# Kernel tuning notes

Measured on AMD Instinct MI355X. Metric: run time of the kernel, lower is better.

The kernel has to match this reference:

```python
import jax, jax.numpy as jnp
import numpy as np

N_NODES = 100000
N_EDGES = 1600000
DIMS = [64, 64, 64, 32]  # in -> hid -> hid -> out


def setup_inputs() -> dict:
    key = jax.random.key(0)
    ks = jax.random.split(key, 12)
    features = jax.random.normal(ks[0], (N_NODES, DIMS[0]), dtype=jnp.float32)
    edge_weights = jax.random.uniform(ks[1], (N_EDGES,), dtype=jnp.float32)
    src = jax.random.randint(ks[2], (N_EDGES,), 0, N_NODES, dtype=jnp.int32)
    dst = jax.random.randint(ks[3], (N_EDGES,), 0, N_NODES, dtype=jnp.int32)
    def lin(kw, kb, i, o):
        s = 1.0 / np.sqrt(i)
        W = jax.random.uniform(kw, (i, o), minval=-s, maxval=s, dtype=jnp.float32)
        b = jax.random.uniform(kb, (o,), minval=-s, maxval=s, dtype=jnp.float32)
        return W, b
    W1, b1 = lin(ks[4], ks[5], DIMS[0], DIMS[1])
    W2, b2 = lin(ks[6], ks[7], DIMS[1], DIMS[2])
    Wp, bp = lin(ks[8], ks[9], DIMS[2], DIMS[3])
    return {"features": features, "edge_weights": edge_weights, "src": src,
            "dst": dst, "W1": W1, "b1": b1, "W2": W2, "b2": b2,
            "Wp": Wp, "bp": bp}


def _graph_conv(x, src, dst, ew, W, b, norm_src, norm_dst):
    # DGL GraphConv, norm='both', with edge weights:
    # h = D_in^{-1/2} * A_w * (D_out^{-1/2} * x) @ W + b
    h = x * norm_src[:, None]
    msg = h[src] * ew[:, None]                      # [E, d] gather + edge-weight
    agg = jax.ops.segment_sum(msg, dst, num_segments=N_NODES)  # scatter-sum
    agg = agg * norm_dst[:, None]
    return agg @ W + b


def reference(features, edge_weights, src, dst, W1, b1, W2, b2, Wp, bp):
    ones = jnp.ones((N_EDGES,), dtype=features.dtype)
    out_deg = jax.ops.segment_sum(ones, src, num_segments=N_NODES)
    in_deg = jax.ops.segment_sum(ones, dst, num_segments=N_NODES)
    norm_src = jnp.power(jnp.clip(out_deg, 1.0, None), -0.5)
    norm_dst = jnp.power(jnp.clip(in_deg, 1.0, None), -0.5)

    x = jax.nn.relu(_graph_conv(features, src, dst, edge_weights, W1, b1, norm_src, norm_dst))
    x = jax.nn.relu(_graph_conv(x, src, dst, edge_weights, W2, b2, norm_src, norm_dst))
    x = _graph_conv(x, src, dst, edge_weights, Wp, bp, norm_src, norm_dst)
    return x
```

## Files before the change

kernel.cpp:

```cpp
#include <hip/hip_runtime.h>

#define N_NODES 100000
#define N_EDGES 1600000
#define NB_SCAN 391
#define NSLICE 64
#define SLICE_E 25000
#define NBUCK 4
#define BUCK_N 25000
#define BUCK_W 12500

__device__ __forceinline__ unsigned short f2bf(float f) {
    unsigned int u = __float_as_uint(f);
    return (unsigned short)((u + 0x7FFFu + ((u >> 16) & 1u)) >> 16);
}
__device__ __forceinline__ float bf2f(unsigned short b) {
    return __uint_as_float(((unsigned int)b) << 16);
}


template <bool RANK>
__global__ void __launch_bounds__(512) count_kernel(
        const int* __restrict__ ids,
        unsigned short* __restrict__ slicecnt,
        unsigned short* __restrict__ rank16) {
    __shared__ unsigned int cnt[BUCK_W];
    int s = blockIdx.x >> 2;
    int b = blockIdx.x & 3;
    int b0 = b * BUCK_N;
    for (int w = threadIdx.x; w < BUCK_W; w += 512) cnt[w] = 0;
    __syncthreads();
    int base = s * SLICE_E;
    for (int i = threadIdx.x; i < SLICE_E; i += 512) {
        int e = base + i;
        int id = ids[e] - b0;
        if ((unsigned)id < (unsigned)BUCK_N) {
            unsigned int shift = (id & 1) * 16;
            unsigned int old = atomicAdd(&cnt[id >> 1], 1u << shift);
            if (RANK) rank16[e] = (unsigned short)((old >> shift) & 0xFFFFu);
        }
    }
    __syncthreads();
    unsigned int* row = (unsigned int*)(slicecnt + (size_t)s * N_NODES) + b * BUCK_W;
    for (int w = threadIdx.x; w < BUCK_W; w += 512) row[w] = cnt[w];
}

__global__ void scan_slices_kernel(unsigned short* __restrict__ scd,
                                   const unsigned short* __restrict__ scs,
                                   int* __restrict__ deg_int,
                                   float* __restrict__ norm_dst,
                                   float* __restrict__ norm_src) {
    int n = blockIdx.x * blockDim.x + threadIdx.x;
    if (n >= N_NODES) return;
    unsigned int tot = 0;
    for (int s = 0; s < NSLICE; ++s) {
        size_t idx = (size_t)s * N_NODES + n;
        unsigned int c = scd[idx];
        scd[idx] = (unsigned short)tot;
        tot += c;
    }
    deg_int[n] = (int)tot;
    norm_dst[n] = rsqrtf(fmaxf((float)tot, 1.0f));
    unsigned int so = 0;
    for (int s = 0; s < NSLICE; ++s) so += scs[(size_t)s * N_NODES + n];
    norm_src[n] = rsqrtf(fmaxf((float)so, 1.0f));
}


__global__ void block_sum_kernel(const int* __restrict__ deg_in, int* __restrict__ block_sums) {
    __shared__ int sdata[256];
    int t = threadIdx.x;
    int n = blockIdx.x * 256 + t;
    int v = (n < N_NODES) ? deg_in[n] : 0;
    sdata[t] = v;
    __syncthreads();
    for (int off = 128; off > 0; off >>= 1) {
        if (t < off) sdata[t] += sdata[t + off];
        __syncthreads();
    }
    if (t == 0) block_sums[blockIdx.x] = sdata[0];
}

__global__ void scan_blocks_kernel(const int* __restrict__ block_sums, int* __restrict__ block_off) {
    __shared__ int part[512];
    int t = threadIdx.x;
    int v = (t < NB_SCAN) ? block_sums[t] : 0;
    part[t] = v;
    __syncthreads();
    for (int off = 1; off < 512; off <<= 1) {
        int u = (t >= off) ? part[t - off] : 0;
        __syncthreads();
        part[t] += u;
        __syncthreads();
    }
    if (t < NB_SCAN) block_off[t] = part[t] - v;
}

__global__ void scatter_rowptr_kernel(const int* __restrict__ deg_in,
                                      const int* __restrict__ block_off,
                                      int* __restrict__ row_ptr) {
    __shared__ int part[256];
    int t = threadIdx.x;
    int n = blockIdx.x * 256 + t;
    int v = (n < N_NODES) ? deg_in[n] : 0;
    part[t] = v;
    __syncthreads();
    for (int off = 1; off < 256; off <<= 1) {
        int u = (t >= off) ? part[t - off] : 0;
        __syncthreads();
        part[t] += u;
        __syncthreads();
    }
    int excl = part[t] - v + block_off[blockIdx.x];
    if (n < N_NODES) row_ptr[n] = excl;
    if (n == N_NODES - 1) row_ptr[N_NODES] = excl + v;
}


__global__ void fill_kernel(const int* __restrict__ src, const int* __restrict__ dst,
                            const float* __restrict__ ew,
                            const float* __restrict__ ns, const float* __restrict__ nd,
                            const int* __restrict__ row_ptr,
                            const unsigned short* __restrict__ sliceoff,
                            const unsigned short* __restrict__ rank16,
                            int2* __restrict__ epack) {
    int i = blockIdx.x * blockDim.x + threadIdx.x;
    int stride = gridDim.x * blockDim.x;
    for (int e = i; e < N_EDGES; e += stride) {
        int s = src[e], d = dst[e];
        int sl = e / SLICE_E;
        int slot = row_ptr[d] + (int)sliceoff[(size_t)sl * N_NODES + d] + (int)rank16[e];
        float c = ns[s] * ew[e] * nd[d];
        epack[slot] = make_int2(s, __float_as_int(c));
    }
}


template <int BM, int DOUT, bool BIAS_RELU>
__global__ void __launch_bounds__(256) matmul_kernel(
        const float* __restrict__ x, const float* __restrict__ W,
        const float* __restrict__ bin, unsigned short* __restrict__ h) {
    constexpr int S = 65;
    constexpr int CG = DOUT / 4;
    __shared__ float Xs[BM * S];
    __shared__ float Ws[64 * DOUT];
    int tid = threadIdx.x;
    int n0 = blockIdx.x * BM;

    for (int i = tid; i < 16 * DOUT; i += 256)
        ((float4*)Ws)[i] = ((const float4*)W)[i];

    float4 bv4;
    if (BIAS_RELU) bv4 = ((const float4*)bin)[tid & 15];
    int c0 = (tid & 15) * 4;
    for (int r = tid >> 4; r < BM; r += 16) {
        int n = n0 + r;
        int nc = n < N_NODES ? n : N_NODES - 1;
        float4 v = ((const float4*)(x + (size_t)nc * 64))[tid & 15];
        if (BIAS_RELU) {
            v.x = fmaxf(v.x + bv4.x, 0.0f);
            v.y = fmaxf(v.y + bv4.y, 0.0f);
            v.z = fmaxf(v.z + bv4.z, 0.0f);
            v.w = fmaxf(v.w + bv4.w, 0.0f);
        }
        Xs[r * S + c0]     = v.x;
        Xs[r * S + c0 + 1] = v.y;
        Xs[r * S + c0 + 2] = v.z;
        Xs[r * S + c0 + 3] = v.w;
    }
    __syncthreads();

    int cg = tid % CG;
    int ng = tid / CG;

    float acc[4][4];
#pragma unroll
    for (int i = 0; i < 4; ++i)
#pragma unroll
        for (int j = 0; j < 4; ++j) acc[i][j] = 0.0f;

#pragma unroll 16
    for (int k = 0; k < 64; ++k) {
        float4 wk = *(const float4*)(&Ws[k * DOUT + cg * 4]);
        float xk[4];
#pragma unroll
        for (int i = 0; i < 4; ++i) xk[i] = Xs[(ng * 4 + i) * S + k];
#pragma unroll
        for (int i = 0; i < 4; ++i) {
            acc[i][0] = fmaf(xk[i], wk.x, acc[i][0]);
            acc[i][1] = fmaf(xk[i], wk.y, acc[i][1]);
            acc[i][2] = fmaf(xk[i], wk.z, acc[i][2]);
            acc[i][3] = fmaf(xk[i], wk.w, acc[i][3]);
        }
    }

#pragma unroll
    for (int i = 0; i < 4; ++i) {
        int n = n0 + ng * 4 + i;
        if (n < N_NODES) {
            ushort4 o;
            o.x = f2bf(acc[i][0]); o.y = f2bf(acc[i][1]);
            o.z = f2bf(acc[i][2]); o.w = f2bf(acc[i][3]);
            *(ushort4*)(&h[(size_t)n * DOUT + cg * 4]) = o;
        }
    }
}


template <int D, bool FINAL>
__global__ void __launch_bounds__(256) csr_agg_kernel(
        const int* __restrict__ row_ptr,
        const int2* __restrict__ epack,
        const unsigned short* __restrict__ h,
        const float* __restrict__ bias, float* __restrict__ out) {
    int tid = blockIdx.x * blockDim.x + threadIdx.x;
    int stride = gridDim.x * blockDim.x;
    int lane = threadIdx.x & (D - 1);
    int node0 = tid / D;
    int nstride = stride / D;
    const unsigned short* hl = h + lane;
    for (int n = node0; n < N_NODES; n += nstride) {
        int s = row_ptr[n];
        int e = row_ptr[n + 1];
        float a0 = 0.f, a1 = 0.f, a2 = 0.f, a3 = 0.f;
        float a4 = 0.f, a5 = 0.f, a6 = 0.f, a7 = 0.f;
        int i = s;
        for (; i + 7 < e; i += 8) {
            int2 p0 = epack[i],     p1 = epack[i + 1], p2 = epack[i + 2], p3 = epack[i + 3];
            int2 p4 = epack[i + 4], p5 = epack[i + 5], p6 = epack[i + 6], p7 = epack[i + 7];
            float h0 = bf2f(hl[(size_t)p0.x * D]);
            float h1 = bf2f(hl[(size_t)p1.x * D]);
            float h2 = bf2f(hl[(size_t)p2.x * D]);
            float h3 = bf2f(hl[(size_t)p3.x * D]);
            float h4 = bf2f(hl[(size_t)p4.x * D]);
            float h5 = bf2f(hl[(size_t)p5.x * D]);
            float h6 = bf2f(hl[(size_t)p6.x * D]);
            float h7 = bf2f(hl[(size_t)p7.x * D]);
            a0 = fmaf(h0, __int_as_float(p0.y), a0);
            a1 = fmaf(h1, __int_as_float(p1.y), a1);
            a2 = fmaf(h2, __int_as_float(p2.y), a2);
            a3 = fmaf(h3, __int_as_float(p3.y), a3);
            a4 = fmaf(h4, __int_as_float(p4.y), a4);
            a5 = fmaf(h5, __int_as_float(p5.y), a5);
            a6 = fmaf(h6, __int_as_float(p6.y), a6);
            a7 = fmaf(h7, __int_as_float(p7.y), a7);
        }
        for (; i + 3 < e; i += 4) {
            int2 p0 = epack[i], p1 = epack[i + 1], p2 = epack[i + 2], p3 = epack[i + 3];
            a0 = fmaf(bf2f(hl[(size_t)p0.x * D]), __int_as_float(p0.y), a0);
            a1 = fmaf(bf2f(hl[(size_t)p1.x * D]), __int_as_float(p1.y), a1);
            a2 = fmaf(bf2f(hl[(size_t)p2.x * D]), __int_as_float(p2.y), a2);
            a3 = fmaf(bf2f(hl[(size_t)p3.x * D]), __int_as_float(p3.y), a3);
        }
        for (; i < e; ++i) {
            int2 p = epack[i];
            a0 = fmaf(bf2f(hl[(size_t)p.x * D]), __int_as_float(p.y), a0);
        }
        float acc = ((a0 + a1) + (a2 + a3)) + ((a4 + a5) + (a6 + a7));
        if (FINAL) out[(size_t)n * D + lane] = acc + bias[lane];
        else       out[(size_t)n * D + lane] = acc;
    }
}

extern "C" void kernel_launch(void* const* d_in, const int* in_sizes, int n_in,
                              void* d_out, int out_size, void* d_ws, size_t ws_size,
                              hipStream_t stream) {
    const float* features = (const float*)d_in[0];
    const float* ew       = (const float*)d_in[1];
    const int*   src      = (const int*)d_in[2];
    const int*   dst      = (const int*)d_in[3];
    const float* W1       = (const float*)d_in[4];
    const float* b1       = (const float*)d_in[5];
    const float* W2       = (const float*)d_in[6];
    const float* b2       = (const float*)d_in[7];
    const float* Wp       = (const float*)d_in[8];
    const float* bp       = (const float*)d_in[9];
    float* out = (float*)d_out;

    float* ws = (float*)d_ws;
    float* norm_src = ws;
    float* norm_dst = ws + 100000;
    int*   deg_int  = (int*)(ws + 200000);
    int*   row_ptr  = (int*)(ws + 300000);
    int*   block_sums = (int*)(ws + 400002);
    int*   block_off  = (int*)(ws + 400394);
    unsigned short* rank16 = (unsigned short*)(ws + 400800);
    int2*  epack = (int2*)(ws + 1200800);
    float* bufA  = ws + 4400800;
    unsigned short* hbuf = (unsigned short*)(ws + 10800800);

    unsigned short* slicecnt_dst = (unsigned short*)bufA;
    unsigned short* slicecnt_src = hbuf;

    count_kernel<true><<<NSLICE * NBUCK, 512, 0, stream>>>(dst, slicecnt_dst, rank16);
    count_kernel<false><<<NSLICE * NBUCK, 512, 0, stream>>>(src, slicecnt_src, nullptr);
    scan_slices_kernel<<<NB_SCAN, 256, 0, stream>>>(slicecnt_dst, slicecnt_src,
                                                    deg_int, norm_dst, norm_src);
    block_sum_kernel<<<NB_SCAN, 256, 0, stream>>>(deg_int, block_sums);
    scan_blocks_kernel<<<1, 512, 0, stream>>>(block_sums, block_off);
    scatter_rowptr_kernel<<<NB_SCAN, 256, 0, stream>>>(deg_int, block_off, row_ptr);
    fill_kernel<<<2048, 256, 0, stream>>>(src, dst, ew, norm_src, norm_dst,
                                          row_ptr, slicecnt_dst, rank16, epack);

    matmul_kernel<64, 64, false><<<1563, 256, 0, stream>>>(features, W1, nullptr, hbuf);
    csr_agg_kernel<64, false><<<4096, 256, 0, stream>>>(row_ptr, epack, hbuf, nullptr, bufA);

    matmul_kernel<64, 64, true><<<1563, 256, 0, stream>>>(bufA, W2, b1, hbuf);
    csr_agg_kernel<64, false><<<4096, 256, 0, stream>>>(row_ptr, epack, hbuf, nullptr, bufA);

    matmul_kernel<128, 32, true><<<782, 256, 0, stream>>>(bufA, Wp, b2, hbuf);
    csr_agg_kernel<32, true><<<4096, 256, 0, stream>>>(row_ptr, epack, hbuf, bp, out);
}
```

Baseline: 307.5 us.

## Fuse CSR aggregation with the following layer's bias, ReLU and matmul

```diff
diff --git a/kernel.cpp b/kernel.cpp
--- a/kernel.cpp
+++ b/kernel.cpp
@@ -135,10 +135,10 @@
 }
 
 
-template <int BM, int DOUT, bool BIAS_RELU>
+template <int BM, int DOUT>
 __global__ void __launch_bounds__(256) matmul_kernel(
         const float* __restrict__ x, const float* __restrict__ W,
-        const float* __restrict__ bin, unsigned short* __restrict__ h) {
+        unsigned short* __restrict__ h) {
     constexpr int S = 65;
     constexpr int CG = DOUT / 4;
     __shared__ float Xs[BM * S];
@@ -149,19 +149,11 @@
     for (int i = tid; i < 16 * DOUT; i += 256)
         ((float4*)Ws)[i] = ((const float4*)W)[i];
 
-    float4 bv4;
-    if (BIAS_RELU) bv4 = ((const float4*)bin)[tid & 15];
     int c0 = (tid & 15) * 4;
     for (int r = tid >> 4; r < BM; r += 16) {
         int n = n0 + r;
         int nc = n < N_NODES ? n : N_NODES - 1;
         float4 v = ((const float4*)(x + (size_t)nc * 64))[tid & 15];
-        if (BIAS_RELU) {
-            v.x = fmaxf(v.x + bv4.x, 0.0f);
-            v.y = fmaxf(v.y + bv4.y, 0.0f);
-            v.z = fmaxf(v.z + bv4.z, 0.0f);
-            v.w = fmaxf(v.w + bv4.w, 0.0f);
-        }
         Xs[r * S + c0]     = v.x;
         Xs[r * S + c0 + 1] = v.y;
         Xs[r * S + c0 + 2] = v.z;
@@ -171,7 +163,6 @@
 
     int cg = tid % CG;
     int ng = tid / CG;
-
     float acc[4][4];
 #pragma unroll
     for (int i = 0; i < 4; ++i)
@@ -206,7 +197,113 @@
 }
 
 
-template <int D, bool FINAL>
+template <int DOUT>
+__global__ void __launch_bounds__(512) agg_mm_kernel(
+        const int* __restrict__ row_ptr,
+        const int2* __restrict__ epack,
+        const unsigned short* __restrict__ hin,
+        const float* __restrict__ bias_in,
+        const float* __restrict__ W,
+        unsigned short* __restrict__ hout) {
+    constexpr int BM = 128;
+    constexpr int S = 65;
+    constexpr int CG = DOUT / 4;
+    constexpr int RI = BM * CG / 512;
+    __shared__ float Xs[BM * S];
+    __shared__ float Ws[64 * DOUT];
+    int tid = threadIdx.x;
+    int n0 = blockIdx.x * BM;
+
+    for (int i = tid; i < 16 * DOUT; i += 512)
+        ((float4*)Ws)[i] = ((const float4*)W)[i];
+
+    int lane = tid & 63;
+    int wid = tid >> 6;
+    float bv = bias_in[lane];
+    const unsigned short* hl = hin + lane;
+
+    for (int j = 0; j < 16; ++j) {
+        int n = n0 + wid * 16 + j;
+        float a0 = 0.f, a1 = 0.f, a2 = 0.f, a3 = 0.f;
+        float a4 = 0.f, a5 = 0.f, a6 = 0.f, a7 = 0.f;
+        if (n < N_NODES) {
+            int s = row_ptr[n];
+            int e = row_ptr[n + 1];
+            int i = s;
+            for (; i + 7 < e; i += 8) {
+                int2 p0 = epack[i],     p1 = epack[i + 1], p2 = epack[i + 2], p3 = epack[i + 3];
+                int2 p4 = epack[i + 4], p5 = epack[i + 5], p6 = epack[i + 6], p7 = epack[i + 7];
+                float h0 = bf2f(hl[(size_t)p0.x * 64]);
+                float h1 = bf2f(hl[(size_t)p1.x * 64]);
+                float h2 = bf2f(hl[(size_t)p2.x * 64]);
+                float h3 = bf2f(hl[(size_t)p3.x * 64]);
+                float h4 = bf2f(hl[(size_t)p4.x * 64]);
+                float h5 = bf2f(hl[(size_t)p5.x * 64]);
+                float h6 = bf2f(hl[(size_t)p6.x * 64]);
+                float h7 = bf2f(hl[(size_t)p7.x * 64]);
+                a0 = fmaf(h0, __int_as_float(p0.y), a0);
+                a1 = fmaf(h1, __int_as_float(p1.y), a1);
+                a2 = fmaf(h2, __int_as_float(p2.y), a2);
+                a3 = fmaf(h3, __int_as_float(p3.y), a3);
+                a4 = fmaf(h4, __int_as_float(p4.y), a4);
+                a5 = fmaf(h5, __int_as_float(p5.y), a5);
+                a6 = fmaf(h6, __int_as_float(p6.y), a6);
+                a7 = fmaf(h7, __int_as_float(p7.y), a7);
+            }
+            for (; i + 3 < e; i += 4) {
+                int2 p0 = epack[i], p1 = epack[i + 1], p2 = epack[i + 2], p3 = epack[i + 3];
+                a0 = fmaf(bf2f(hl[(size_t)p0.x * 64]), __int_as_float(p0.y), a0);
+                a1 = fmaf(bf2f(hl[(size_t)p1.x * 64]), __int_as_float(p1.y), a1);
+                a2 = fmaf(bf2f(hl[(size_t)p2.x * 64]), __int_as_float(p2.y), a2);
+                a3 = fmaf(bf2f(hl[(size_t)p3.x * 64]), __int_as_float(p3.y), a3);
+            }
+            for (; i < e; ++i) {
+                int2 p = epack[i];
+                a0 = fmaf(bf2f(hl[(size_t)p.x * 64]), __int_as_float(p.y), a0);
+            }
+        }
+        float acc = ((a0 + a1) + (a2 + a3)) + ((a4 + a5) + (a6 + a7));
+        Xs[(wid * 16 + j) * S + lane] = fmaxf(acc + bv, 0.0f);
+    }
+    __syncthreads();
+
+    int cg = tid % CG;
+    int ng = tid / CG;
+    float acc[RI][4];
+#pragma unroll
+    for (int i = 0; i < RI; ++i)
+#pragma unroll
+        for (int j = 0; j < 4; ++j) acc[i][j] = 0.0f;
+
+#pragma unroll 16
+    for (int k = 0; k < 64; ++k) {
+        float4 wk = *(const float4*)(&Ws[k * DOUT + cg * 4]);
+        float xk[RI];
+#pragma unroll
+        for (int i = 0; i < RI; ++i) xk[i] = Xs[(ng * RI + i) * S + k];
+#pragma unroll
+        for (int i = 0; i < RI; ++i) {
+            acc[i][0] = fmaf(xk[i], wk.x, acc[i][0]);
+            acc[i][1] = fmaf(xk[i], wk.y, acc[i][1]);
+            acc[i][2] = fmaf(xk[i], wk.z, acc[i][2]);
+            acc[i][3] = fmaf(xk[i], wk.w, acc[i][3]);
+        }
+    }
+
+#pragma unroll
+    for (int i = 0; i < RI; ++i) {
+        int n = n0 + ng * RI + i;
+        if (n < N_NODES) {
+            ushort4 o;
+            o.x = f2bf(acc[i][0]); o.y = f2bf(acc[i][1]);
+            o.z = f2bf(acc[i][2]); o.w = f2bf(acc[i][3]);
+            *(ushort4*)(&hout[(size_t)n * DOUT + cg * 4]) = o;
+        }
+    }
+}
+
+
+template <int D>
 __global__ void __launch_bounds__(256) csr_agg_kernel(
         const int* __restrict__ row_ptr,
         const int2* __restrict__ epack,
@@ -227,22 +324,14 @@
         for (; i + 7 < e; i += 8) {
             int2 p0 = epack[i],     p1 = epack[i + 1], p2 = epack[i + 2], p3 = epack[i + 3];
             int2 p4 = epack[i + 4], p5 = epack[i + 5], p6 = epack[i + 6], p7 = epack[i + 7];
-            float h0 = bf2f(hl[(size_t)p0.x * D]);
-            float h1 = bf2f(hl[(size_t)p1.x * D]);
-            float h2 = bf2f(hl[(size_t)p2.x * D]);
-            float h3 = bf2f(hl[(size_t)p3.x * D]);
-            float h4 = bf2f(hl[(size_t)p4.x * D]);
-            float h5 = bf2f(hl[(size_t)p5.x * D]);
-            float h6 = bf2f(hl[(size_t)p6.x * D]);
-            float h7 = bf2f(hl[(size_t)p7.x * D]);
-            a0 = fmaf(h0, __int_as_float(p0.y), a0);
-            a1 = fmaf(h1, __int_as_float(p1.y), a1);
-            a2 = fmaf(h2, __int_as_float(p2.y), a2);
-            a3 = fmaf(h3, __int_as_float(p3.y), a3);
-            a4 = fmaf(h4, __int_as_float(p4.y), a4);
-            a5 = fmaf(h5, __int_as_float(p5.y), a5);
-            a6 = fmaf(h6, __int_as_float(p6.y), a6);
-            a7 = fmaf(h7, __int_as_float(p7.y), a7);
+            a0 = fmaf(bf2f(hl[(size_t)p0.x * D]), __int_as_float(p0.y), a0);
+            a1 = fmaf(bf2f(hl[(size_t)p1.x * D]), __int_as_float(p1.y), a1);
+            a2 = fmaf(bf2f(hl[(size_t)p2.x * D]), __int_as_float(p2.y), a2);
+            a3 = fmaf(bf2f(hl[(size_t)p3.x * D]), __int_as_float(p3.y), a3);
+            a4 = fmaf(bf2f(hl[(size_t)p4.x * D]), __int_as_float(p4.y), a4);
+            a5 = fmaf(bf2f(hl[(size_t)p5.x * D]), __int_as_float(p5.y), a5);
+            a6 = fmaf(bf2f(hl[(size_t)p6.x * D]), __int_as_float(p6.y), a6);
+            a7 = fmaf(bf2f(hl[(size_t)p7.x * D]), __int_as_float(p7.y), a7);
         }
         for (; i + 3 < e; i += 4) {
             int2 p0 = epack[i], p1 = epack[i + 1], p2 = epack[i + 2], p3 = epack[i + 3];
@@ -256,8 +345,7 @@
             a0 = fmaf(bf2f(hl[(size_t)p.x * D]), __int_as_float(p.y), a0);
         }
         float acc = ((a0 + a1) + (a2 + a3)) + ((a4 + a5) + (a6 + a7));
-        if (FINAL) out[(size_t)n * D + lane] = acc + bias[lane];
-        else       out[(size_t)n * D + lane] = acc;
+        out[(size_t)n * D + lane] = acc + bias[lane];
     }
 }
 
@@ -285,11 +373,11 @@
     int*   block_off  = (int*)(ws + 400394);
     unsigned short* rank16 = (unsigned short*)(ws + 400800);
     int2*  epack = (int2*)(ws + 1200800);
-    float* bufA  = ws + 4400800;
-    unsigned short* hbuf = (unsigned short*)(ws + 10800800);
-
-    unsigned short* slicecnt_dst = (unsigned short*)bufA;
-    unsigned short* slicecnt_src = hbuf;
+    unsigned short* hbufA = (unsigned short*)(ws + 4400800);
+    unsigned short* hbufB = (unsigned short*)(ws + 10800800);
+
+    unsigned short* slicecnt_dst = hbufA;
+    unsigned short* slicecnt_src = hbufB;
 
     count_kernel<true><<<NSLICE * NBUCK, 512, 0, stream>>>(dst, slicecnt_dst, rank16);
     count_kernel<false><<<NSLICE * NBUCK, 512, 0, stream>>>(src, slicecnt_src, nullptr);
@@ -301,12 +389,11 @@
     fill_kernel<<<2048, 256, 0, stream>>>(src, dst, ew, norm_src, norm_dst,
                                           row_ptr, slicecnt_dst, rank16, epack);
 
-    matmul_kernel<64, 64, false><<<1563, 256, 0, stream>>>(features, W1, nullptr, hbuf);
-    csr_agg_kernel<64, false><<<4096, 256, 0, stream>>>(row_ptr, epack, hbuf, nullptr, bufA);
-
-    matmul_kernel<64, 64, true><<<1563, 256, 0, stream>>>(bufA, W2, b1, hbuf);
-    csr_agg_kernel<64, false><<<4096, 256, 0, stream>>>(row_ptr, epack, hbuf, nullptr, bufA);
-
-    matmul_kernel<128, 32, true><<<782, 256, 0, stream>>>(bufA, Wp, b2, hbuf);
-    csr_agg_kernel<32, true><<<4096, 256, 0, stream>>>(row_ptr, epack, hbuf, bp, out);
-}
+    matmul_kernel<64, 64><<<1563, 256, 0, stream>>>(features, W1, hbufA);
+
+    agg_mm_kernel<64><<<782, 512, 0, stream>>>(row_ptr, epack, hbufA, b1, W2, hbufB);
+
+    agg_mm_kernel<32><<<782, 512, 0, stream>>>(row_ptr, epack, hbufB, b2, Wp, hbufA);
+
+    csr_agg_kernel<32><<<4096, 256, 0, stream>>>(row_ptr, epack, hbufA, bp, out);
+}
```

Result: slower. 375.7 us (+22.2%).

## Pack edges into 32-bit words with quantized weights and move norms out of edges

Applied to the files above, without the earlier changes.

```diff
diff --git a/kernel.cpp b/kernel.cpp
--- a/kernel.cpp
+++ b/kernel.cpp
@@ -47,7 +47,7 @@
 __global__ void scan_slices_kernel(unsigned short* __restrict__ scd,
                                    const unsigned short* __restrict__ scs,
                                    int* __restrict__ deg_int,
-                                   float* __restrict__ norm_dst,
+                                   float* __restrict__ ndq,
                                    float* __restrict__ norm_src) {
     int n = blockIdx.x * blockDim.x + threadIdx.x;
     if (n >= N_NODES) return;
@@ -59,7 +59,7 @@
         tot += c;
     }
     deg_int[n] = (int)tot;
-    norm_dst[n] = rsqrtf(fmaxf((float)tot, 1.0f));
+    ndq[n] = rsqrtf(fmaxf((float)tot, 1.0f)) * (1.0f / 32767.0f);
     unsigned int so = 0;
     for (int s = 0; s < NSLICE; ++s) so += scs[(size_t)s * N_NODES + n];
     norm_src[n] = rsqrtf(fmaxf((float)so, 1.0f));
@@ -118,19 +118,18 @@
 
 __global__ void fill_kernel(const int* __restrict__ src, const int* __restrict__ dst,
                             const float* __restrict__ ew,
-                            const float* __restrict__ ns, const float* __restrict__ nd,
                             const int* __restrict__ row_ptr,
                             const unsigned short* __restrict__ sliceoff,
                             const unsigned short* __restrict__ rank16,
-                            int2* __restrict__ epack) {
+                            unsigned int* __restrict__ epack) {
     int i = blockIdx.x * blockDim.x + threadIdx.x;
     int stride = gridDim.x * blockDim.x;
     for (int e = i; e < N_EDGES; e += stride) {
         int s = src[e], d = dst[e];
         int sl = e / SLICE_E;
         int slot = row_ptr[d] + (int)sliceoff[(size_t)sl * N_NODES + d] + (int)rank16[e];
-        float c = ns[s] * ew[e] * nd[d];
-        epack[slot] = make_int2(s, __float_as_int(c));
+        unsigned int q = (unsigned int)(ew[e] * 32767.0f + 0.5f);
+        epack[slot] = ((unsigned int)s << 15) | q;
     }
 }
 
@@ -138,7 +137,8 @@
 template <int BM, int DOUT, bool BIAS_RELU>
 __global__ void __launch_bounds__(256) matmul_kernel(
         const float* __restrict__ x, const float* __restrict__ W,
-        const float* __restrict__ bin, unsigned short* __restrict__ h) {
+        const float* __restrict__ bin, const float* __restrict__ ns,
+        unsigned short* __restrict__ h) {
     constexpr int S = 65;
     constexpr int CG = DOUT / 4;
     __shared__ float Xs[BM * S];
@@ -171,7 +171,6 @@
 
     int cg = tid % CG;
     int ng = tid / CG;
-
     float acc[4][4];
 #pragma unroll
     for (int i = 0; i < 4; ++i)
@@ -197,9 +196,10 @@
     for (int i = 0; i < 4; ++i) {
         int n = n0 + ng * 4 + i;
         if (n < N_NODES) {
+            float nsv = ns[n];
             ushort4 o;
-            o.x = f2bf(acc[i][0]); o.y = f2bf(acc[i][1]);
-            o.z = f2bf(acc[i][2]); o.w = f2bf(acc[i][3]);
+            o.x = f2bf(acc[i][0] * nsv); o.y = f2bf(acc[i][1] * nsv);
+            o.z = f2bf(acc[i][2] * nsv); o.w = f2bf(acc[i][3] * nsv);
             *(ushort4*)(&h[(size_t)n * DOUT + cg * 4]) = o;
         }
     }
@@ -209,8 +209,9 @@
 template <int D, bool FINAL>
 __global__ void __launch_bounds__(256) csr_agg_kernel(
         const int* __restrict__ row_ptr,
-        const int2* __restrict__ epack,
+        const unsigned int* __restrict__ epack,
         const unsigned short* __restrict__ h,
+        const float* __restrict__ ndq,
         const float* __restrict__ bias, float* __restrict__ out) {
     int tid = blockIdx.x * blockDim.x + threadIdx.x;
     int stride = gridDim.x * blockDim.x;
@@ -225,37 +226,37 @@
         float a4 = 0.f, a5 = 0.f, a6 = 0.f, a7 = 0.f;
         int i = s;
         for (; i + 7 < e; i += 8) {
-            int2 p0 = epack[i],     p1 = epack[i + 1], p2 = epack[i + 2], p3 = epack[i + 3];
-            int2 p4 = epack[i + 4], p5 = epack[i + 5], p6 = epack[i + 6], p7 = epack[i + 7];
-            float h0 = bf2f(hl[(size_t)p0.x * D]);
-            float h1 = bf2f(hl[(size_t)p1.x * D]);
-            float h2 = bf2f(hl[(size_t)p2.x * D]);
-            float h3 = bf2f(hl[(size_t)p3.x * D]);
-            float h4 = bf2f(hl[(size_t)p4.x * D]);
-            float h5 = bf2f(hl[(size_t)p5.x * D]);
-            float h6 = bf2f(hl[(size_t)p6.x * D]);
-            float h7 = bf2f(hl[(size_t)p7.x * D]);
-            a0 = fmaf(h0, __int_as_float(p0.y), a0);
-            a1 = fmaf(h1, __int_as_float(p1.y), a1);
-            a2 = fmaf(h2, __int_as_float(p2.y), a2);
-            a3 = fmaf(h3, __int_as_float(p3.y), a3);
-            a4 = fmaf(h4, __int_as_float(p4.y), a4);
-            a5 = fmaf(h5, __int_as_float(p5.y), a5);
-            a6 = fmaf(h6, __int_as_float(p6.y), a6);
-            a7 = fmaf(h7, __int_as_float(p7.y), a7);
+            unsigned int p0 = epack[i],     p1 = epack[i + 1], p2 = epack[i + 2], p3 = epack[i + 3];
+            unsigned int p4 = epack[i + 4], p5 = epack[i + 5], p6 = epack[i + 6], p7 = epack[i + 7];
+            float h0 = bf2f(hl[(size_t)(p0 >> 15) * D]);
+            float h1 = bf2f(hl[(size_t)(p1 >> 15) * D]);
+            float h2 = bf2f(hl[(size_t)(p2 >> 15) * D]);
+            float h3 = bf2f(hl[(size_t)(p3 >> 15) * D]);
+            float h4 = bf2f(hl[(size_t)(p4 >> 15) * D]);
+            float h5 = bf2f(hl[(size_t)(p5 >> 15) * D]);
+            float h6 = bf2f(hl[(size_t)(p6 >> 15) * D]);
+            float h7 = bf2f(hl[(size_t)(p7 >> 15) * D]);
+            a0 = fmaf((float)(p0 & 32767u), h0, a0);
+            a1 = fmaf((float)(p1 & 32767u), h1, a1);
+            a2 = fmaf((float)(p2 & 32767u), h2, a2);
+            a3 = fmaf((float)(p3 & 32767u), h3, a3);
+            a4 = fmaf((float)(p4 & 32767u), h4, a4);
+            a5 = fmaf((float)(p5 & 32767u), h5, a5);
+            a6 = fmaf((float)(p6 & 32767u), h6, a6);
+            a7 = fmaf((float)(p7 & 32767u), h7, a7);
         }
         for (; i + 3 < e; i += 4) {
-            int2 p0 = epack[i], p1 = epack[i + 1], p2 = epack[i + 2], p3 = epack[i + 3];
-            a0 = fmaf(bf2f(hl[(size_t)p0.x * D]), __int_as_float(p0.y), a0);
-            a1 = fmaf(bf2f(hl[(size_t)p1.x * D]), __int_as_float(p1.y), a1);
-            a2 = fmaf(bf2f(hl[(size_t)p2.x * D]), __int_as_float(p2.y), a2);
-            a3 = fmaf(bf2f(hl[(size_t)p3.x * D]), __int_as_float(p3.y), a3);
+            unsigned int p0 = epack[i], p1 = epack[i + 1], p2 = epack[i + 2], p3 = epack[i + 3];
+            a0 = fmaf((float)(p0 & 32767u), bf2f(hl[(size_t)(p0 >> 15) * D]), a0);
+            a1 = fmaf((float)(p1 & 32767u), bf2f(hl[(size_t)(p1 >> 15) * D]), a1);
+            a2 = fmaf((float)(p2 & 32767u), bf2f(hl[(size_t)(p2 >> 15) * D]), a2);
+            a3 = fmaf((float)(p3 & 32767u), bf2f(hl[(size_t)(p3 >> 15) * D]), a3);
         }
         for (; i < e; ++i) {
-            int2 p = epack[i];
-            a0 = fmaf(bf2f(hl[(size_t)p.x * D]), __int_as_float(p.y), a0);
-        }
-        float acc = ((a0 + a1) + (a2 + a3)) + ((a4 + a5) + (a6 + a7));
+            unsigned int p = epack[i];
+            a0 = fmaf((float)(p & 32767u), bf2f(hl[(size_t)(p >> 15) * D]), a0);
+        }
+        float acc = (((a0 + a1) + (a2 + a3)) + ((a4 + a5) + (a6 + a7))) * ndq[n];
         if (FINAL) out[(size_t)n * D + lane] = acc + bias[lane];
         else       out[(size_t)n * D + lane] = acc;
     }
@@ -278,35 +279,35 @@
 
     float* ws = (float*)d_ws;
     float* norm_src = ws;
-    float* norm_dst = ws + 100000;
+    float* ndq      = ws + 100000;
     int*   deg_int  = (int*)(ws + 200000);
     int*   row_ptr  = (int*)(ws + 300000);
     int*   block_sums = (int*)(ws + 400002);
     int*   block_off  = (int*)(ws + 400394);
     unsigned short* rank16 = (unsigned short*)(ws + 400800);
-    int2*  epack = (int2*)(ws + 1200800);
-    float* bufA  = ws + 4400800;
-    unsigned short* hbuf = (unsigned short*)(ws + 10800800);
-
-    unsigned short* slicecnt_dst = (unsigned short*)bufA;
-    unsigned short* slicecnt_src = hbuf;
+    unsigned int*   epack  = (unsigned int*)(ws + 1200800);
+    unsigned short* hbuf   = (unsigned short*)(ws + 2800800);
+    float*          bufA   = ws + 6000800;
+
+    unsigned short* slicecnt_dst = hbuf;
+    unsigned short* slicecnt_src = (unsigned short*)bufA;
 
     count_kernel<true><<<NSLICE * NBUCK, 512, 0, stream>>>(dst, slicecnt_dst, rank16);
     count_kernel<false><<<NSLICE * NBUCK, 512, 0, stream>>>(src, slicecnt_src, nullptr);
     scan_slices_kernel<<<NB_SCAN, 256, 0, stream>>>(slicecnt_dst, slicecnt_src,
-                                                    deg_int, norm_dst, norm_src);
+                                                    deg_int, ndq, norm_src);
     block_sum_kernel<<<NB_SCAN, 256, 0, stream>>>(deg_int, block_sums);
     scan_blocks_kernel<<<1, 512, 0, stream>>>(block_sums, block_off);
     scatter_rowptr_kernel<<<NB_SCAN, 256, 0, stream>>>(deg_int, block_off, row_ptr);
-    fill_kernel<<<2048, 256, 0, stream>>>(src, dst, ew, norm_src, norm_dst,
-                                          row_ptr, slicecnt_dst, rank16, epack);
-
-    matmul_kernel<64, 64, false><<<1563, 256, 0, stream>>>(features, W1, nullptr, hbuf);
-    csr_agg_kernel<64, false><<<4096, 256, 0, stream>>>(row_ptr, epack, hbuf, nullptr, bufA);
-
-    matmul_kernel<64, 64, true><<<1563, 256, 0, stream>>>(bufA, W2, b1, hbuf);
-    csr_agg_kernel<64, false><<<4096, 256, 0, stream>>>(row_ptr, epack, hbuf, nullptr, bufA);
-
-    matmul_kernel<128, 32, true><<<782, 256, 0, stream>>>(bufA, Wp, b2, hbuf);
-    csr_agg_kernel<32, true><<<4096, 256, 0, stream>>>(row_ptr, epack, hbuf, bp, out);
-}
+    fill_kernel<<<2048, 256, 0, stream>>>(src, dst, ew, row_ptr,
+                                          slicecnt_dst, rank16, epack);
+
+    matmul_kernel<64, 64, false><<<1563, 256, 0, stream>>>(features, W1, nullptr, norm_src, hbuf);
+    csr_agg_kernel<64, false><<<4096, 256, 0, stream>>>(row_ptr, epack, hbuf, ndq, nullptr, bufA);
+
+    matmul_kernel<64, 64, true><<<1563, 256, 0, stream>>>(bufA, W2, b1, norm_src, hbuf);
+    csr_agg_kernel<64, false><<<4096, 256, 0, stream>>>(row_ptr, epack, hbuf, ndq, nullptr, bufA);
+
+    matmul_kernel<128, 32, true><<<782, 256, 0, stream>>>(bufA, Wp, b2, norm_src, hbuf);
+    csr_agg_kernel<32, true><<<4096, 256, 0, stream>>>(row_ptr, epack, hbuf, ndq, bp, out);
+}
```

After: 289.7 us. 1.06x faster.
